# Kernel optimization log

Measured on AMD Instinct MI355X. Metric: run time of the kernel, lower is better.

Reference implementation:

```python
import jax, jax.numpy as jnp
import numpy as np

B, N, C, H, P = 8, 4096, 512, 8, 64
D = C // H


def setup_inputs() -> dict:
    key = jax.random.key(0)
    ks = jax.random.split(key, 5)
    s = 0.02
    return {
        "x": jax.random.normal(ks[0], (B, N, C), jnp.float32),
        "w_qkv": jax.random.normal(ks[1], (3 * C, C), jnp.float32) * s,
        "w_e": jax.random.normal(ks[2], (P, N), jnp.float32) * s,
        "b_e": jnp.zeros((P,), jnp.float32),
        "temperature": jnp.ones((1, 1, 1), jnp.float32),
        "temperature2": jnp.ones((H, 1, 1), jnp.float32),
        "w_o1": jax.random.normal(ks[3], (C // 2, C), jnp.float32) * s,
        "b_o1": jnp.zeros((C // 2,), jnp.float32),
        "w_o2": jax.random.normal(ks[4], (C // 2, C), jnp.float32) * s,
        "b_o2": jnp.zeros((C // 2,), jnp.float32),
    }


def reference(x, w_qkv, w_e, b_e, temperature, temperature2, w_o1, b_o1, w_o2, b_o2):
    Bs, Ns, Cs = x.shape
    # qkvv projection and head split: [B,N,3C] -> [3,B,H,N,D]
    qkv = (x @ w_qkv.T).reshape(Bs, Ns, 3, H, D)
    qkv = jnp.transpose(qkv, (2, 0, 3, 1, 4))
    q, k, v = qkv[0], qkv[1], qkv[2]
    q_t = jnp.swapaxes(q, -2, -1)  # [B,H,D,N]
    k_t = jnp.swapaxes(k, -2, -1)  # [B,H,D,N]
    v_t = jnp.swapaxes(v, -2, -1)  # [B,H,D,N]
    # Linformer-style projection along token axis; E = F (shared weights)
    kp = k_t @ w_e.T + b_e  # [B,H,D,P]
    vp = v_t @ w_e.T + b_e  # [B,H,D,P]
    # L2-normalize q along tokens (k is normalized in the original AFTER
    # projection, so that normalization is dead code and omitted)
    qn = q_t / jnp.maximum(jnp.linalg.norm(q_t, axis=-1, keepdims=True), 1e-12)
    # ---- channel attention: [B,C,C] scores over raw x ----
    xt = jnp.swapaxes(x, -2, -1)  # [B,C,N]
    attn_ca = jax.nn.softmax((xt @ x) * temperature, axis=-1)
    x_ca = jnp.swapaxes(attn_ca @ xt, -2, -1)  # [B,N,C]
    # ---- projected spatial attention: [B,H,N,P] scores ----
    attn_sa = jax.nn.softmax(
        jnp.einsum('bhdn,bhdp->bhnp', qn, kp) * temperature2, axis=-1)
    x_sa = jnp.einsum('bhnp,bhdp->bhnd', attn_sa, vp)  # [B,H,N,D]
    # faithful to torch: permute(0,3,1,2) then reshape(B,N,C)
    x_sa = jnp.transpose(x_sa, (0, 3, 1, 2)).reshape(Bs, Ns, Cs)
    out = jnp.concatenate(
        [x_sa @ w_o1.T + b_o1, x_ca @ w_o2.T + b_o2], axis=-1)
    return out
```

## Files before the change

kernel.cpp:

```cpp
#include <hip/hip_runtime.h>
#include <hip/hip_bf16.h>

typedef unsigned short u16;

#define AS1 __attribute__((address_space(1)))
#define AS3 __attribute__((address_space(3)))

static __device__ __forceinline__ float bl(u16 v) {
    return __uint_as_float(((unsigned)v) << 16);
}
static __device__ __forceinline__ u16 f2b(float f) {
    unsigned u = __float_as_uint(f);
    unsigned r = u + 0x7FFFu + ((u >> 16) & 1u);
    return (u16)(r >> 16);
}
static __device__ __forceinline__ float ldf(const void* p, long i, int isbf) {
    if (isbf) return bl(((const u16*)p)[i]);
    return ((const float*)p)[i];
}
static __device__ __forceinline__ void gload_lds16(const u16* g, u16* l) {
    __builtin_amdgcn_global_load_lds((const AS1 void*)g, (AS3 void*)l, 16, 0, 0);
}

typedef __attribute__((ext_vector_type(8))) short bf16x8;
typedef __attribute__((ext_vector_type(4))) float f32x4;

static __device__ __forceinline__ bf16x8 pack8(const float* p) {
    const float4 x0 = ((const float4*)p)[0];
    const float4 x1 = ((const float4*)p)[1];
    unsigned r0, r1, r2, r3;
    asm("v_cvt_pk_bf16_f32 %0, %1, %2" : "=v"(r0) : "v"(x0.x), "v"(x0.y));
    asm("v_cvt_pk_bf16_f32 %0, %1, %2" : "=v"(r1) : "v"(x0.z), "v"(x0.w));
    asm("v_cvt_pk_bf16_f32 %0, %1, %2" : "=v"(r2) : "v"(x1.x), "v"(x1.y));
    asm("v_cvt_pk_bf16_f32 %0, %1, %2" : "=v"(r3) : "v"(x1.z), "v"(x1.w));
    union { unsigned u[4]; bf16x8 v; } u;
    u.u[0] = r0; u.u[1] = r1; u.u[2] = r2; u.u[3] = r3;
    return u.v;
}

__global__ void dtype_probe(const void* __restrict__ temp, unsigned* __restrict__ flag) {
    if (threadIdx.x == 0 && blockIdx.x == 0)
        flag[0] = (((const u16*)temp)[0] == 0x3F80) ? 1u : 0u;
}

__global__ __launch_bounds__(256) void zero_f32(float* __restrict__ p, long n) {
    const long stride = (long)gridDim.x * 256;
    for (long i = (long)blockIdx.x * 256 + threadIdx.x; i < n; i += stride)
        p[i] = 0.f;
}

__global__ __launch_bounds__(256) void conv_x(const void* __restrict__ X,
                                              u16* __restrict__ xb,
                                              u16* __restrict__ xt,
                                              const unsigned* __restrict__ flg)
{
    __shared__ u16 tile[64][65];
    const int f = (int)flg[0];
    const int b = blockIdx.z;
    const int n0 = blockIdx.x * 64, c0 = blockIdx.y * 64;
    const int t = threadIdx.x, r0 = t >> 6, c = t & 63;
    #pragma unroll
    for (int rr = 0; rr < 16; ++rr) {
        const int r = rr * 4 + r0;
        const long gi = ((long)b * 4096 + n0 + r) * 512 + c0 + c;
        const u16 h = f2b(ldf(X, gi, f));
        xb[gi] = h;
        tile[r][c] = h;
    }
    __syncthreads();
    #pragma unroll
    for (int rr = 0; rr < 16; ++rr) {
        const int cc = rr * 4 + r0;
        xt[((long)b * 512 + c0 + cc) * 4096 + n0 + c] = tile[c][cc];
    }
}

__global__ __launch_bounds__(256) void conv_w(const void* __restrict__ W,
                                              u16* __restrict__ wb, long nelem,
                                              const unsigned* __restrict__ flg)
{
    const int f = (int)flg[0];
    const long stride = (long)gridDim.x * 256;
    for (long i = (long)blockIdx.x * 256 + threadIdx.x; i < nelem; i += stride)
        wb[i] = f2b(ldf(W, i, f));
}

__global__ __launch_bounds__(256) void gemm_mfma_nt(
    const u16* __restrict__ A, const u16* __restrict__ B,
    void* __restrict__ C, const void* __restrict__ bias,
    int M, int N, int K, int lda, int ldb, int ldc,
    long sA, long sB, long sC,
    const unsigned* __restrict__ flg, int biasExt, int cF32, int kSplit,
    float* __restrict__ qsq)
{
    __shared__ u16 Asm[128 * 32];
    __shared__ u16 Bsm[128 * 32];
    const int t = threadIdx.x, w = t >> 6, l = t & 63;
    int bz = blockIdx.z, kz = 0;
    if (kSplit > 1) { kz = bz % kSplit; bz = bz / kSplit; }
    const u16* Ab = A + (long)bz * sA;
    const u16* Bb = B + (long)bz * sB;
    const int m0 = blockIdx.x * 128, n0 = blockIdx.y * 128;
    const int wm = (w >> 1) * 64, wn = (w & 1) * 64;
    const int srow = l >> 2;
    const int scol = (l & 3) * 8;
    const int fr = l & 15;
    const int fk = (l >> 4) * 8;
    f32x4 acc[4][4];
    #pragma unroll
    for (int i = 0; i < 4; ++i)
        #pragma unroll
        for (int j = 0; j < 4; ++j)
            acc[i][j] = (f32x4){0.f, 0.f, 0.f, 0.f};

    const int kChunk = K / kSplit;
    const int kBeg = kz * kChunk, kEnd = kBeg + kChunk;
    for (int k0 = kBeg; k0 < kEnd; k0 += 32) {
        __syncthreads();
        {
            const int q0 = w, q1 = w + 4;
            gload_lds16(Ab + (long)(m0 + q0 * 16 + srow) * lda + k0 + scol, &Asm[q0 * 512]);
            gload_lds16(Ab + (long)(m0 + q1 * 16 + srow) * lda + k0 + scol, &Asm[q1 * 512]);
            gload_lds16(Bb + (long)(n0 + q0 * 16 + srow) * ldb + k0 + scol, &Bsm[q0 * 512]);
            gload_lds16(Bb + (long)(n0 + q1 * 16 + srow) * ldb + k0 + scol, &Bsm[q1 * 512]);
        }
        __syncthreads();
        bf16x8 af[4], bf[4];
        #pragma unroll
        for (int i = 0; i < 4; ++i) {
            af[i] = *(const bf16x8*)&Asm[(wm + i * 16 + fr) * 32 + fk];
            bf[i] = *(const bf16x8*)&Bsm[(wn + i * 16 + fr) * 32 + fk];
        }
        #pragma unroll
        for (int i = 0; i < 4; ++i)
            #pragma unroll
            for (int j = 0; j < 4; ++j)
                acc[i][j] = __builtin_amdgcn_mfma_f32_16x16x32_bf16(af[i], bf[j], acc[i][j], 0, 0, 0);
    }
    const int f = (int)flg[0];
    const long cOff = (long)bz * sC;
    float bj[4] = {0.f, 0.f, 0.f, 0.f};
    if (bias) {
        #pragma unroll
        for (int j = 0; j < 4; ++j)
            bj[j] = ldf(bias, n0 + wn + j * 16 + fr, biasExt ? f : 1);
    }
    #pragma unroll
    for (int i = 0; i < 4; ++i) {
        #pragma unroll
        for (int j = 0; j < 4; ++j) {
            const int col = n0 + wn + j * 16 + fr;
            #pragma unroll
            for (int r = 0; r < 4; ++r) {
                const int row = m0 + wm + i * 16 + (l >> 4) * 4 + r;
                const float v = acc[i][j][r] + bj[j];
                if (kSplit > 1)
                    atomicAdd(&((float*)C)[cOff + (long)row * ldc + col], v);
                else if (cF32)
                    ((float*)C)[cOff + (long)row * ldc + col] = v;
                else
                    ((u16*)C)[cOff + (long)row * ldc + col] = f2b(v);
            }
        }
    }
    if (qsq) {
        #pragma unroll
        for (int j = 0; j < 4; ++j) {
            const int col = n0 + wn + j * 16 + fr;
            if (col < 512) {
                float s = 0.f;
                #pragma unroll
                for (int i = 0; i < 4; ++i)
                    #pragma unroll
                    for (int r = 0; r < 4; ++r)
                        s = fmaf(acc[i][j][r], acc[i][j][r], s);
                s += __shfl_xor(s, 16, 64);
                s += __shfl_xor(s, 32, 64);
                if ((l >> 4) == 0)
                    atomicAdd(&qsq[(long)bz * 512 + col], s);
            }
        }
    }
}

__global__ __launch_bounds__(256) void xe_mfma(const u16* __restrict__ WEB,
                                               const u16* __restrict__ XT,
                                               float* __restrict__ XE)
{
    const int t = threadIdx.x, w = t >> 6, l = t & 63;
    const int l15 = l & 15, g = l >> 4;
    const int c0 = blockIdx.x * 128 + (w >> 1) * 64;
    const int b = blockIdx.y;
    const int nbase = blockIdx.z * 512 + (w & 1) * 256;
    f32x4 acc[4][4];
    #pragma unroll
    for (int i = 0; i < 4; ++i)
        #pragma unroll
        for (int j = 0; j < 4; ++j)
            acc[i][j] = (f32x4){0.f, 0.f, 0.f, 0.f};
    for (int ks = 0; ks < 8; ++ks) {
        const int n = nbase + ks * 32 + g * 8;
        bf16x8 a[4], bb[4];
        #pragma unroll
        for (int i = 0; i < 4; ++i)
            a[i] = *(const bf16x8*)&WEB[(long)(i * 16 + l15) * 4096 + n];
        #pragma unroll
        for (int j = 0; j < 4; ++j)
            bb[j] = *(const bf16x8*)&XT[((long)b * 512 + c0 + j * 16 + l15) * 4096 + n];
        #pragma unroll
        for (int i = 0; i < 4; ++i)
            #pragma unroll
            for (int j = 0; j < 4; ++j)
                acc[i][j] = __builtin_amdgcn_mfma_f32_16x16x32_bf16(a[i], bb[j], acc[i][j], 0, 0, 0);
    }
    #pragma unroll
    for (int i = 0; i < 4; ++i)
        #pragma unroll
        for (int j = 0; j < 4; ++j)
            #pragma unroll
            for (int r = 0; r < 4; ++r)
                atomicAdd(&XE[((long)b * 64 + i * 16 + g * 4 + r) * 512 + c0 + j * 16 + l15],
                          acc[i][j][r]);
}

__global__ __launch_bounds__(256) void kpvp2_mfma(const float* __restrict__ XE,
                                                  const u16* __restrict__ WQB,
                                                  const float* __restrict__ qsq,
                                                  const void* __restrict__ be,
                                                  const void* __restrict__ temp2,
                                                  u16* __restrict__ kpT,
                                                  u16* __restrict__ vpB,
                                                  const unsigned* __restrict__ flg)
{
    __shared__ float lds[4][4096];
    const int bh = blockIdx.x, b = bh >> 3, h = bh & 7;
    const int t = threadIdx.x, w = t >> 6, l = t & 63;
    const int l15 = l & 15, g = l >> 4;
    const int isV = w >> 1;
    const int ch = w & 1;
    const u16* wrow = WQB + (long)(512 + isV * 512 + h * 64) * 512;
    const float* xr = XE + (long)b * 64 * 512;
    f32x4 acc[4][4];
    #pragma unroll
    for (int i = 0; i < 4; ++i)
        #pragma unroll
        for (int j = 0; j < 4; ++j)
            acc[i][j] = (f32x4){0.f, 0.f, 0.f, 0.f};
    for (int ks = 0; ks < 8; ++ks) {
        const int c = ch * 256 + ks * 32 + g * 8;
        bf16x8 a[4], bb[4];
        if (!isV) {
            #pragma unroll
            for (int i = 0; i < 4; ++i)
                a[i] = pack8(&xr[(long)(i * 16 + l15) * 512 + c]);
            #pragma unroll
            for (int j = 0; j < 4; ++j)
                bb[j] = *(const bf16x8*)&wrow[(long)(j * 16 + l15) * 512 + c];
        } else {
            #pragma unroll
            for (int i = 0; i < 4; ++i)
                a[i] = *(const bf16x8*)&wrow[(long)(i * 16 + l15) * 512 + c];
            #pragma unroll
            for (int j = 0; j < 4; ++j)
                bb[j] = pack8(&xr[(long)(j * 16 + l15) * 512 + c]);
        }
        #pragma unroll
        for (int i = 0; i < 4; ++i)
            #pragma unroll
            for (int j = 0; j < 4; ++j)
                acc[i][j] = __builtin_amdgcn_mfma_f32_16x16x32_bf16(a[i], bb[j], acc[i][j], 0, 0, 0);
    }
    #pragma unroll
    for (int i = 0; i < 4; ++i)
        #pragma unroll
        for (int j = 0; j < 4; ++j)
            #pragma unroll
            for (int r = 0; r < 4; ++r)
                lds[w][(i * 16 + g * 4 + r) * 64 + j * 16 + l15] = acc[i][j][r];
    __syncthreads();
    const int f = (int)flg[0];
    if (t < 128) {
        const float t2 = ldf(temp2, h, f);
        for (int e = t; e < 4096; e += 128) {
            const int p = e >> 6, d = e & 63;
            const float rn = 1.0f / fmaxf(sqrtf(qsq[b * 512 + h * 64 + d]), 1e-12f);
            kpT[(long)bh * 4096 + e] = f2b((lds[0][e] + lds[1][e] + ldf(be, p, f)) * rn * t2);
        }
    } else {
        for (int e = t - 128; e < 4096; e += 128) {
            vpB[(long)bh * 4096 + e] = f2b(lds[2][e] + lds[3][e] + ldf(be, e & 63, f));
        }
    }
}

__global__ __launch_bounds__(256) void softmax_ca(const float* __restrict__ S,
                                                  u16* __restrict__ A,
                                                  const void* __restrict__ temp,
                                                  const unsigned* __restrict__ flg)
{
    __shared__ float red[256];
    const int row = blockIdx.x;
    const int t = threadIdx.x;
    const float tv = ldf(temp, 0, (int)flg[0]);
    const float* s = S + (long)row * 512;
    float v0 = s[t] * tv;
    float v1 = s[t + 256] * tv;
    red[t] = fmaxf(v0, v1);
    __syncthreads();
    for (int o = 128; o > 0; o >>= 1) {
        if (t < o) red[t] = fmaxf(red[t], red[t + o]);
        __syncthreads();
    }
    const float m = red[0];
    __syncthreads();
    float e0 = expf(v0 - m), e1 = expf(v1 - m);
    red[t] = e0 + e1;
    __syncthreads();
    for (int o = 128; o > 0; o >>= 1) {
        if (t < o) red[t] += red[t + o];
        __syncthreads();
    }
    const float inv = 1.0f / red[0];
    u16* a = A + (long)row * 512;
    a[t]       = f2b(e0 * inv);
    a[t + 256] = f2b(e1 * inv);
}

__global__ __launch_bounds__(256) void spatial_attn_mfma(
    const u16* __restrict__ Q, const u16* __restrict__ kpT,
    const u16* __restrict__ vpB, u16* __restrict__ XSA)
{
    __shared__ u16 P[4][4096];
    const int bh = blockIdx.y, b = bh >> 3, h = bh & 7;
    const int t = threadIdx.x, w = t >> 6, l = t & 63;
    const int l15 = l & 15, g = l >> 4;
    const int n0 = blockIdx.x * 256 + w * 64;
    char* Pw = (char*)&P[w][0];

    const u16* kb = kpT + (long)bh * 4096;
    const u16* vb = vpB + (long)bh * 4096;
    bf16x8 akp[2][4], avp[2][4];
    #pragma unroll
    for (int ks = 0; ks < 2; ++ks)
        #pragma unroll
        for (int i = 0; i < 4; ++i) {
            akp[ks][i] = *(const bf16x8*)&kb[(i * 16 + l15) * 64 + ks * 32 + g * 8];
            avp[ks][i] = *(const bf16x8*)&vb[(i * 16 + l15) * 64 + ks * 32 + g * 8];
        }

    f32x4 sacc[4][4];
    #pragma unroll
    for (int i = 0; i < 4; ++i)
        #pragma unroll
        for (int j = 0; j < 4; ++j)
            sacc[i][j] = (f32x4){0.f, 0.f, 0.f, 0.f};
    const u16* qb = Q + ((long)b * 4096 + n0) * 512 + h * 64;
    #pragma unroll
    for (int ks = 0; ks < 2; ++ks) {
        bf16x8 bq[4];
        #pragma unroll
        for (int j = 0; j < 4; ++j)
            bq[j] = *(const bf16x8*)&qb[(long)(j * 16 + l15) * 512 + ks * 32 + g * 8];
        #pragma unroll
        for (int i = 0; i < 4; ++i)
            #pragma unroll
            for (int j = 0; j < 4; ++j)
                sacc[i][j] = __builtin_amdgcn_mfma_f32_16x16x32_bf16(akp[ks][i], bq[j], sacc[i][j], 0, 0, 0);
    }

    #pragma unroll
    for (int j = 0; j < 4; ++j) {
        float m = sacc[0][j][0];
        #pragma unroll
        for (int i = 0; i < 4; ++i)
            #pragma unroll
            for (int r = 0; r < 4; ++r)
                m = fmaxf(m, sacc[i][j][r]);
        m = fmaxf(m, __shfl_xor(m, 16, 64));
        m = fmaxf(m, __shfl_xor(m, 32, 64));
        float s = 0.f;
        #pragma unroll
        for (int i = 0; i < 4; ++i)
            #pragma unroll
            for (int r = 0; r < 4; ++r) {
                const float e = __expf(sacc[i][j][r] - m);
                sacc[i][j][r] = e;
                s += e;
            }
        s += __shfl_xor(s, 16, 64);
        s += __shfl_xor(s, 32, 64);
        const float inv = 1.0f / s;
        const int n = j * 16 + l15;
        const int swz = (n & 7) << 4;
        #pragma unroll
        for (int i = 0; i < 4; ++i) {
            unsigned lo, hi;
            float p0 = sacc[i][j][0] * inv, p1 = sacc[i][j][1] * inv;
            float p2 = sacc[i][j][2] * inv, p3 = sacc[i][j][3] * inv;
            asm("v_cvt_pk_bf16_f32 %0, %1, %2" : "=v"(lo) : "v"(p0), "v"(p1));
            asm("v_cvt_pk_bf16_f32 %0, %1, %2" : "=v"(hi) : "v"(p2), "v"(p3));
            const int byte = (n * 128 + i * 32 + g * 8) ^ swz;
            *(uint2*)(Pw + byte) = make_uint2(lo, hi);
        }
    }

    f32x4 oacc[4][4];
    #pragma unroll
    for (int i = 0; i < 4; ++i)
        #pragma unroll
        for (int j = 0; j < 4; ++j)
            oacc[i][j] = (f32x4){0.f, 0.f, 0.f, 0.f};
    #pragma unroll
    for (int ks = 0; ks < 2; ++ks) {
        bf16x8 bp[4];
        #pragma unroll
        for (int j = 0; j < 4; ++j) {
            const int n = j * 16 + l15;
            const int byte = (n * 128 + ks * 64 + g * 16) ^ ((n & 7) << 4);
            bp[j] = *(const bf16x8*)(Pw + byte);
        }
        #pragma unroll
        for (int i = 0; i < 4; ++i)
            #pragma unroll
            for (int j = 0; j < 4; ++j)
                oacc[i][j] = __builtin_amdgcn_mfma_f32_16x16x32_bf16(avp[ks][i], bp[j], oacc[i][j], 0, 0, 0);
    }

    const int rowoff = h * 8 + (n0 >> 9);
    const int colbase = n0 & 511;
    #pragma unroll
    for (int i = 0; i < 4; ++i)
        #pragma unroll
        for (int r = 0; r < 4; ++r) {
            const int d = i * 16 + g * 4 + r;
            u16* orow = XSA + ((long)b * 4096 + d * 64 + rowoff) * 512 + colbase;
            #pragma unroll
            for (int j = 0; j < 4; ++j)
                orow[j * 16 + l15] = f2b(oacc[i][j][r]);
        }
}

extern "C" void kernel_launch(void* const* d_in, const int* in_sizes, int n_in,
                              void* d_out, int out_size, void* d_ws, size_t ws_size,
                              hipStream_t stream)
{
    const void* x     = d_in[0];
    const void* w_qkv = d_in[1];
    const void* w_e   = d_in[2];
    const void* b_e   = d_in[3];
    const void* temp  = d_in[4];
    const void* temp2 = d_in[5];
    const void* w_o1  = d_in[6];
    const void* b_o1  = d_in[7];
    const void* w_o2  = d_in[8];
    const void* b_o2  = d_in[9];
    float* out = (float*)d_out;

    char* ws = (char*)d_ws;
    unsigned* flag = (unsigned*)ws; ws += 256;
    u16*   qb     = (u16*)ws;   ws += (size_t)8 * 4096 * 512 * 2;
    float* qsq    = (float*)ws; ws += (size_t)4096 * 4;
    float* xe     = (float*)ws; ws += (size_t)8 * 64 * 512 * 4;
    float* scores = (float*)ws; ws += (size_t)8 * 512 * 512 * 4;
    u16*   attn   = (u16*)ws;   ws += (size_t)8 * 512 * 512 * 2;
    u16*   x_ca   = (u16*)ws;   ws += (size_t)8 * 4096 * 512 * 2;
    u16*   xt     = (u16*)ws;   ws += (size_t)8 * 512 * 4096 * 2;
    u16*   xb     = (u16*)ws;   ws += (size_t)8 * 4096 * 512 * 2;
    u16*   wqb    = (u16*)ws;   ws += (size_t)1536 * 512 * 2;
    u16*   web    = (u16*)ws;   ws += (size_t)64 * 4096 * 2;
    u16*   wo1b   = (u16*)ws;   ws += (size_t)256 * 512 * 2;
    u16*   wo2b   = (u16*)ws;   ws += (size_t)256 * 512 * 2;
    u16*   kpT    = (u16*)ws;   ws += (size_t)262144 * 2;
    u16*   vpB    = (u16*)ws;   ws += (size_t)262144 * 2;
    u16*   x_sa   = xt;

    dtype_probe<<<1, 64, 0, stream>>>(temp, flag);
    conv_x<<<dim3(64, 8, 8), 256, 0, stream>>>(x, xb, xt, flag);
    conv_w<<<768, 256, 0, stream>>>(w_qkv, wqb, 1536L * 512, flag);
    conv_w<<<128, 256, 0, stream>>>(w_e, web, 64L * 4096, flag);
    conv_w<<<128, 256, 0, stream>>>(w_o1, wo1b, 256L * 512, flag);
    conv_w<<<128, 256, 0, stream>>>(w_o2, wo2b, 256L * 512, flag);
    zero_f32<<<4, 256, 0, stream>>>(qsq, 4096);
    gemm_mfma_nt<<<dim3(32, 4, 8), 256, 0, stream>>>(
        xb, wqb, qb, nullptr, 4096, 512, 512, 512, 512, 512,
        (long)4096 * 512, 0, (long)4096 * 512, flag, 0, 0, 1, qsq);
    zero_f32<<<128, 256, 0, stream>>>(xe, (long)8 * 64 * 512);
    xe_mfma<<<dim3(4, 8, 8), 256, 0, stream>>>(web, xt, xe);
    kpvp2_mfma<<<64, 256, 0, stream>>>(xe, wqb, qsq, b_e, temp2, kpT, vpB, flag);
    zero_f32<<<2048, 256, 0, stream>>>(scores, (long)8 * 512 * 512);
    gemm_mfma_nt<<<dim3(4, 4, 32), 256, 0, stream>>>(
        xt, xt, scores, nullptr, 512, 512, 4096, 4096, 4096, 512,
        (long)512 * 4096, (long)512 * 4096, (long)512 * 512, flag, 0, 1, 4, nullptr);
    softmax_ca<<<4096, 256, 0, stream>>>(scores, attn, temp, flag);
    gemm_mfma_nt<<<dim3(32, 4, 8), 256, 0, stream>>>(
        xb, attn, x_ca, nullptr, 4096, 512, 512, 512, 512, 512,
        (long)4096 * 512, (long)512 * 512, (long)4096 * 512, flag, 0, 0, 1, nullptr);
    spatial_attn_mfma<<<dim3(16, 64), 256, 0, stream>>>(qb, kpT, vpB, x_sa);
    gemm_mfma_nt<<<dim3(32, 2, 8), 256, 0, stream>>>(
        x_sa, wo1b, out, b_o1, 4096, 256, 512, 512, 512, 512,
        (long)4096 * 512, 0, (long)4096 * 512, flag, 1, 1, 1, nullptr);
    gemm_mfma_nt<<<dim3(32, 2, 8), 256, 0, stream>>>(
        x_ca, wo2b, out + 256, b_o2, 4096, 256, 512, 512, 512, 512,
        (long)4096 * 512, 0, (long)4096 * 512, flag, 1, 1, 1, nullptr);
}
```

Before: 404.5 us.

## Double-buffer LDS tiles in MFMA GEMM and remap workgroups across XCDs

The GEMM main loop now uses two LDS buffers, issuing the global-to-LDS loads for the next K-tile before running the MFMAs on the current one, with a single barrier per iteration instead of two. This is meant to hide global load latency behind compute. The block index is also remapped so consecutive linear workgroup IDs are spread across the 8 XCDs, which is intended to improve L2 locality for neighbouring tiles. LDS use doubles, which could lower occupancy. The prefetch also relies on the asynchronous LDS loads completing before the barrier.

```diff
diff --git a/kernel.cpp b/kernel.cpp
--- a/kernel.cpp
+++ b/kernel.cpp
@@ -93,14 +93,22 @@
     const unsigned* __restrict__ flg, int biasExt, int cF32, int kSplit,
     float* __restrict__ qsq)
 {
-    __shared__ u16 Asm[128 * 32];
-    __shared__ u16 Bsm[128 * 32];
+    __shared__ u16 Asm[2][128 * 32];
+    __shared__ u16 Bsm[2][128 * 32];
     const int t = threadIdx.x, w = t >> 6, l = t & 63;
-    int bz = blockIdx.z, kz = 0;
-    if (kSplit > 1) { kz = bz % kSplit; bz = bz / kSplit; }
+    const int gx = gridDim.x, gy = gridDim.y;
+    const long nwg = (long)gx * gy * gridDim.z;
+    const long lin = blockIdx.x + (long)gx * (blockIdx.y + (long)gy * blockIdx.z);
+    long nid = lin;
+    if ((nwg & 7) == 0) nid = (lin & 7) * (nwg >> 3) + (lin >> 3);
+    const int by = (int)(nid % gy);
+    const long r2 = nid / gy;
+    const int bx = (int)(r2 % gx);
+    int bz = (int)(r2 / gx), kz = 0;
+    if (kSplit > 1) { kz = bz % kSplit; bz /= kSplit; }
     const u16* Ab = A + (long)bz * sA;
     const u16* Bb = B + (long)bz * sB;
-    const int m0 = blockIdx.x * 128, n0 = blockIdx.y * 128;
+    const int m0 = bx * 128, n0 = by * 128;
     const int wm = (w >> 1) * 64, wn = (w & 1) * 64;
     const int srow = l >> 2;
     const int scol = (l & 3) * 8;
@@ -115,28 +123,37 @@
 
     const int kChunk = K / kSplit;
     const int kBeg = kz * kChunk, kEnd = kBeg + kChunk;
+    const int q0 = w, q1 = w + 4;
+
+#define STAGE(nb, kk)                                                                   \
+    do {                                                                                \
+        gload_lds16(Ab + (long)(m0 + q0 * 16 + srow) * lda + (kk) + scol, &Asm[nb][q0 * 512]); \
+        gload_lds16(Ab + (long)(m0 + q1 * 16 + srow) * lda + (kk) + scol, &Asm[nb][q1 * 512]); \
+        gload_lds16(Bb + (long)(n0 + q0 * 16 + srow) * ldb + (kk) + scol, &Bsm[nb][q0 * 512]); \
+        gload_lds16(Bb + (long)(n0 + q1 * 16 + srow) * ldb + (kk) + scol, &Bsm[nb][q1 * 512]); \
+    } while (0)
+
+    STAGE(0, kBeg);
+    __syncthreads();
+    int cur = 0;
     for (int k0 = kBeg; k0 < kEnd; k0 += 32) {
+        if (k0 + 32 < kEnd) STAGE(cur ^ 1, k0 + 32);
+        bf16x8 af[4], bf[4];
+        #pragma unroll
+        for (int i = 0; i < 4; ++i) {
+            af[i] = *(const bf16x8*)&Asm[cur][(wm + i * 16 + fr) * 32 + fk];
+            bf[i] = *(const bf16x8*)&Bsm[cur][(wn + i * 16 + fr) * 32 + fk];
+        }
+        #pragma unroll
+        for (int i = 0; i < 4; ++i)
+            #pragma unroll
+            for (int j = 0; j < 4; ++j)
+                acc[i][j] = __builtin_amdgcn_mfma_f32_16x16x32_bf16(af[i], bf[j], acc[i][j], 0, 0, 0);
         __syncthreads();
-        {
-            const int q0 = w, q1 = w + 4;
-            gload_lds16(Ab + (long)(m0 + q0 * 16 + srow) * lda + k0 + scol, &Asm[q0 * 512]);
-            gload_lds16(Ab + (long)(m0 + q1 * 16 + srow) * lda + k0 + scol, &Asm[q1 * 512]);
-            gload_lds16(Bb + (long)(n0 + q0 * 16 + srow) * ldb + k0 + scol, &Bsm[q0 * 512]);
-            gload_lds16(Bb + (long)(n0 + q1 * 16 + srow) * ldb + k0 + scol, &Bsm[q1 * 512]);
-        }
-        __syncthreads();
-        bf16x8 af[4], bf[4];
-        #pragma unroll
-        for (int i = 0; i < 4; ++i) {
-            af[i] = *(const bf16x8*)&Asm[(wm + i * 16 + fr) * 32 + fk];
-            bf[i] = *(const bf16x8*)&Bsm[(wn + i * 16 + fr) * 32 + fk];
-        }
-        #pragma unroll
-        for (int i = 0; i < 4; ++i)
-            #pragma unroll
-            for (int j = 0; j < 4; ++j)
-                acc[i][j] = __builtin_amdgcn_mfma_f32_16x16x32_bf16(af[i], bf[j], acc[i][j], 0, 0, 0);
-    }
+        cur ^= 1;
+    }
+#undef STAGE
+
     const int f = (int)flg[0];
     const long cOff = (long)bz * sC;
     float bj[4] = {0.f, 0.f, 0.f, 0.f};
```

Measured after the change: 398.9 us. Within noise of the previous version (-1.4%).
